# Optimization experiments

Measured on AMD Instinct MI355X. Metric: run time of the kernel, lower is better.

## Reference

```python
import jax, jax.numpy as jnp
import numpy as np

N, E, IN_DIM, H, D = 100000, 1600000, 256, 4, 32


def setup_inputs() -> dict:
    key = jax.random.key(0)
    ks = jax.random.split(key, 12)
    glorot = lambda k, shp: jax.random.normal(k, shp, dtype=jnp.float32) * np.float32(np.sqrt(2.0 / (shp[0] + shp[1])))
    return {
        "x": jax.random.normal(ks[0], (N, IN_DIM), dtype=jnp.float32),
        "row": jnp.sort(jax.random.randint(ks[1], (E,), 0, N)),
        "col": jax.random.randint(ks[2], (E,), 0, N),
        "a1_w": glorot(ks[3], (H, IN_DIM)),
        "a1_b": jnp.zeros((H,), jnp.float32),
        "a2_w": glorot(ks[4], (H, IN_DIM)),
        "a2_b": jnp.zeros((H,), jnp.float32),
        "lin_l_w": glorot(ks[5], (H * D, IN_DIM)),
        "lin_l_b": jnp.zeros((H * D,), jnp.float32),
        "lin_r_w": glorot(ks[6], (H * D, IN_DIM)),
        "lin_r_b": jnp.zeros((H * D,), jnp.float32),
    }


def reference(x, row, col, a1_w, a1_b, a2_w, a2_b, lin_l_w, lin_l_b, lin_r_w, lin_r_b):
    n = x.shape[0]
    # per-node attention logits, gathered per edge: attn[e,h] = a1(x)[row[e],h] + a2(x)[col[e],h]
    attn1 = x @ a1_w.T + a1_b            # [N, H]
    attn2 = x @ a2_w.T + a2_b            # [N, H]
    attn = attn1[row] + attn2[col]       # [E, H]
    # segment softmax over destination node (row), numerically stable
    seg_max = jax.ops.segment_max(attn, row, num_segments=n)
    seg_max = jnp.where(jnp.isfinite(seg_max), seg_max, 0.0)  # isolated nodes
    e = jnp.exp(attn - seg_max[row])
    seg_sum = jax.ops.segment_sum(e, row, num_segments=n)
    attn_d = e / (seg_sum[row] + 1e-16)  # [E, H]
    # per-head sparse weighted aggregation: out[r] += attn_d[e] * xw[col[e]]
    xw = (x @ lin_l_w.T + lin_l_b).reshape(n, H, D)
    msg = attn_d[:, :, None] * xw[col]   # [E, H, D]
    out_l = jax.ops.segment_sum(msg, row, num_segments=n).reshape(n, H * D)
    return out_l + x @ lin_r_w.T + lin_r_b
```

## Files before the change

### kernel.cpp

```cpp
#include <hip/hip_runtime.h>
#include <hip/hip_bf16.h>
#include <math.h>

#define IN_DIM 256
#define NH 4
#define HD 128

typedef __attribute__((ext_vector_type(8))) short short8;
typedef __attribute__((ext_vector_type(4))) float floatx4;
typedef __attribute__((ext_vector_type(2))) float floatx2;

__device__ __forceinline__ unsigned short f2bf(float f) {
    __hip_bfloat16 h = __float2bfloat16(f);
    return *reinterpret_cast<unsigned short*>(&h);
}
__device__ __forceinline__ float asf(unsigned int u) {
    union { unsigned int i; float f; } c; c.i = u; return c.f;
}

__global__ __launch_bounds__(256) void build_rowptr_k(const int* __restrict__ row,
                                                      int* __restrict__ rowptr,
                                                      int E, int N) {
    int e = blockIdx.x * blockDim.x + threadIdx.x;
    if (e >= E) return;
    int r = row[e];
    int rprev = (e > 0) ? row[e - 1] : -1;
    for (int rr = rprev + 1; rr <= r; ++rr) rowptr[rr] = e;
    if (e == E - 1) {
        for (int rr = r + 1; rr <= N; ++rr) rowptr[rr] = E;
    }
}

__global__ __launch_bounds__(256) void prep_w_k(const float* __restrict__ ll_w,
                                                const float* __restrict__ lr_w,
                                                unsigned short* __restrict__ Wb) {
    int idx = blockIdx.x * 256 + threadIdx.x;
    int j = idx >> 8, k = idx & 255;
    float v = (j < 128) ? ll_w[(size_t)j * 256 + k] : lr_w[(size_t)(j - 128) * 256 + k];
    Wb[idx] = f2bf(v);
}

__global__ __launch_bounds__(256) void attn_conv_k(
    const float* __restrict__ x,
    const float* __restrict__ a2_w, const float* __restrict__ a2_b,
    float* __restrict__ eattn, unsigned short* __restrict__ xb, int N)
{
    const int n = blockIdx.x * 4 + (threadIdx.x >> 6);
    const int lane = threadIdx.x & 63;
    if (n >= N) return;
    const float4 xv = ((const float4*)x)[(size_t)n * 64 + lane];
    ushort4 pk;
    pk.x = f2bf(xv.x); pk.y = f2bf(xv.y); pk.z = f2bf(xv.z); pk.w = f2bf(xv.w);
    *(ushort4*)(xb + (size_t)n * IN_DIM + lane * 4) = pk;
    #pragma unroll
    for (int c = 0; c < 4; ++c) {
        const float4 wv = ((const float4*)(a2_w + (size_t)c * IN_DIM))[lane];
        float p = xv.x * wv.x + xv.y * wv.y + xv.z * wv.z + xv.w * wv.w;
        #pragma unroll
        for (int o = 32; o; o >>= 1) p += __shfl_xor(p, o, 64);
        if (lane == 0) eattn[(size_t)n * NH + c] = __expf(p + a2_b[c]);
    }
}

__global__ __launch_bounds__(512, 4) void node_gemm_k(
    const unsigned short* __restrict__ xb, const unsigned short* __restrict__ Wb,
    const float* __restrict__ ll_b, const float* __restrict__ lr_b,
    unsigned short* __restrict__ xwb, float* __restrict__ out, int N)
{
    __shared__ unsigned short Abuf[2][32 * 264];
    __shared__ unsigned short LdsX[32 * 136];
    __shared__ float          LdsO[32 * 132];

    const int tid = threadIdx.x;
    const int lane = tid & 63;
    const int w = tid >> 6;
    const int lo = lane & 15;
    const int hi = lane >> 4;

    short8 Bf[2][8];
    int cols[2]; float bias[2];
    #pragma unroll
    for (int ct = 0; ct < 2; ++ct) {
        const int col = w * 32 + ct * 16 + lo;
        cols[ct] = col;
        bias[ct] = (col < HD) ? ll_b[col] : lr_b[col - HD];
        #pragma unroll
        for (int s = 0; s < 8; ++s)
            Bf[ct][s] = *(const short8*)(Wb + (size_t)col * IN_DIM + s * 32 + hi * 8);
    }

    const int tr = tid >> 4;
    const int tk = (tid & 15) * 16;

    uint4 st0, st1;
    auto gload = [&](int slab) {
        int rg = slab * 32 + tr;
        if (rg >= N) rg = 0;
        const uint4* p = (const uint4*)(xb + (size_t)rg * IN_DIM + tk);
        st0 = p[0]; st1 = p[1];
    };

    const int nslab = (N + 31) >> 5;
    int slab = blockIdx.x;
    gload(slab);
    int pb = 0;

    for (; slab < nslab; slab += gridDim.x) {
        unsigned short* ab = &Abuf[pb][0];
        *(uint4*)(ab + tr * 264 + tk) = st0;
        *(uint4*)(ab + tr * 264 + tk + 8) = st1;
        __syncthreads();

        const int next = slab + gridDim.x;
        if (next < nslab) gload(next);

        floatx4 acc[2][2];
        #pragma unroll
        for (int rt = 0; rt < 2; ++rt)
            #pragma unroll
            for (int ct = 0; ct < 2; ++ct)
                acc[rt][ct] = (floatx4){0.f, 0.f, 0.f, 0.f};

        #pragma unroll
        for (int s = 0; s < 8; ++s) {
            const short8 A0 = *(const short8*)(ab + lo * 264 + s * 32 + hi * 8);
            const short8 A1 = *(const short8*)(ab + (16 + lo) * 264 + s * 32 + hi * 8);
            acc[0][0] = __builtin_amdgcn_mfma_f32_16x16x32_bf16(A0, Bf[0][s], acc[0][0], 0, 0, 0);
            acc[0][1] = __builtin_amdgcn_mfma_f32_16x16x32_bf16(A0, Bf[1][s], acc[0][1], 0, 0, 0);
            acc[1][0] = __builtin_amdgcn_mfma_f32_16x16x32_bf16(A1, Bf[0][s], acc[1][0], 0, 0, 0);
            acc[1][1] = __builtin_amdgcn_mfma_f32_16x16x32_bf16(A1, Bf[1][s], acc[1][1], 0, 0, 0);
        }

        #pragma unroll
        for (int rt = 0; rt < 2; ++rt)
            #pragma unroll
            for (int ct = 0; ct < 2; ++ct) {
                const int c = cols[ct];
                #pragma unroll
                for (int j = 0; j < 4; ++j) {
                    const int r = rt * 16 + hi * 4 + j;
                    const float v = acc[rt][ct][j] + bias[ct];
                    if (c < HD) LdsX[r * 136 + c] = f2bf(v);
                    else        LdsO[r * 132 + (c - HD)] = v;
                }
            }

        asm volatile("s_waitcnt lgkmcnt(0)\n\ts_barrier" ::: "memory");

        {
            const int rg = slab * 32 + tr;
            if (rg < N) {
                *(uint4*)(xwb + (size_t)rg * HD + (tid & 15) * 8) =
                    *(const uint4*)(LdsX + tr * 136 + (tid & 15) * 8);
                float4* od = (float4*)(out + (size_t)rg * HD + (tid & 15) * 8);
                const float* lsrc = LdsO + tr * 132 + (tid & 15) * 8;
                od[0] = *(const float4*)(lsrc);
                od[1] = *(const float4*)(lsrc + 4);
            }
        }
        pb ^= 1;
    }
}

__global__ __launch_bounds__(256) void edge_aggregate_k(
    const int* __restrict__ rowptr, const int* __restrict__ col,
    const float* __restrict__ eattn,
    const unsigned short* __restrict__ xwb, float* __restrict__ out, int N)
{
    const int n = blockIdx.x * 4 + (threadIdx.x >> 6);
    const int lane = threadIdx.x & 63;
    if (n >= N) return;
    const int e0 = __builtin_amdgcn_readfirstlane(rowptr[n]);
    const int e1 = __builtin_amdgcn_readfirstlane(rowptr[n + 1]);
    if (e0 >= e1) return;

    const int h = lane >> 4;
    const int d2 = 2 * lane;

    floatx2* op = (floatx2*)(out + (size_t)n * HD + d2);
    floatx2 o = __builtin_nontemporal_load(op);

    float s = 0.f, acc0 = 0.f, acc1 = 0.f;
    int e = e0;

    if (e + 4 <= e1) {
        int c0 = col[e], c1 = col[e + 1], c2 = col[e + 2], c3 = col[e + 3];
        for (; e + 8 <= e1; e += 4) {
            const float w0 = eattn[c0 * NH + h];
            const float w1 = eattn[c1 * NH + h];
            const float w2 = eattn[c2 * NH + h];
            const float w3 = eattn[c3 * NH + h];
            const unsigned int p0 = *(const unsigned int*)(xwb + c0 * HD + d2);
            const unsigned int p1 = *(const unsigned int*)(xwb + c1 * HD + d2);
            const unsigned int p2 = *(const unsigned int*)(xwb + c2 * HD + d2);
            const unsigned int p3 = *(const unsigned int*)(xwb + c3 * HD + d2);
            const int n0 = col[e + 4];
            const int n1 = col[e + 5];
            const int n2 = col[e + 6];
            const int n3 = col[e + 7];
            s += (w0 + w1) + (w2 + w3);
            acc0 += w0 * asf(p0 << 16) + w1 * asf(p1 << 16);
            acc0 += w2 * asf(p2 << 16) + w3 * asf(p3 << 16);
            acc1 += w0 * asf(p0 & 0xffff0000u) + w1 * asf(p1 & 0xffff0000u);
            acc1 += w2 * asf(p2 & 0xffff0000u) + w3 * asf(p3 & 0xffff0000u);
            c0 = n0; c1 = n1; c2 = n2; c3 = n3;
        }
        {
            const float w0 = eattn[c0 * NH + h];
            const float w1 = eattn[c1 * NH + h];
            const float w2 = eattn[c2 * NH + h];
            const float w3 = eattn[c3 * NH + h];
            const unsigned int p0 = *(const unsigned int*)(xwb + c0 * HD + d2);
            const unsigned int p1 = *(const unsigned int*)(xwb + c1 * HD + d2);
            const unsigned int p2 = *(const unsigned int*)(xwb + c2 * HD + d2);
            const unsigned int p3 = *(const unsigned int*)(xwb + c3 * HD + d2);
            s += (w0 + w1) + (w2 + w3);
            acc0 += w0 * asf(p0 << 16) + w1 * asf(p1 << 16);
            acc0 += w2 * asf(p2 << 16) + w3 * asf(p3 << 16);
            acc1 += w0 * asf(p0 & 0xffff0000u) + w1 * asf(p1 & 0xffff0000u);
            acc1 += w2 * asf(p2 & 0xffff0000u) + w3 * asf(p3 & 0xffff0000u);
            e += 4;
        }
    }
    for (; e < e1; ++e) {
        const int c0 = col[e];
        const float w0 = eattn[c0 * NH + h];
        const unsigned int p0 = *(const unsigned int*)(xwb + c0 * HD + d2);
        s += w0;
        acc0 += w0 * asf(p0 << 16);
        acc1 += w0 * asf(p0 & 0xffff0000u);
    }

    const float inv = 1.f / s;
    o.x += acc0 * inv;
    o.y += acc1 * inv;
    __builtin_nontemporal_store(o, op);
}

extern "C" void kernel_launch(void* const* d_in, const int* in_sizes, int n_in,
                              void* d_out, int out_size, void* d_ws, size_t ws_size,
                              hipStream_t stream) {
    const float* x    = (const float*)d_in[0];
    const int*   row  = (const int*)d_in[1];
    const int*   col  = (const int*)d_in[2];
    const float* a2_w = (const float*)d_in[5];
    const float* a2_b = (const float*)d_in[6];
    const float* ll_w = (const float*)d_in[7];
    const float* ll_b = (const float*)d_in[8];
    const float* lr_w = (const float*)d_in[9];
    const float* lr_b = (const float*)d_in[10];
    float* out = (float*)d_out;

    const int N = in_sizes[0] / IN_DIM;
    const int E = in_sizes[1];

    char* ws = (char*)d_ws;
    size_t off = ((size_t)(N + 1) * sizeof(int) + 255) & ~(size_t)255;
    int*   rowptr = (int*)ws;
    float* eattn  = (float*)(ws + off); off += (size_t)N * NH * sizeof(float);
    unsigned short* xwb = (unsigned short*)(ws + off); off += (size_t)N * HD * sizeof(unsigned short);
    unsigned short* Wb  = (unsigned short*)(ws + off); off += (size_t)256 * IN_DIM * sizeof(unsigned short);
    unsigned short* xb  = (unsigned short*)(ws + off); off += (size_t)N * IN_DIM * sizeof(unsigned short);

    prep_w_k<<<256, 256, 0, stream>>>(ll_w, lr_w, Wb);
    build_rowptr_k<<<(E + 255) / 256, 256, 0, stream>>>(row, rowptr, E, N);
    attn_conv_k<<<(N + 3) / 4, 256, 0, stream>>>(x, a2_w, a2_b, eattn, xb, N);
    node_gemm_k<<<512, 512, 0, stream>>>(xb, Wb, ll_b, lr_b, xwb, out, N);
    edge_aggregate_k<<<(N + 3) / 4, 256, 0, stream>>>(rowptr, col, eattn, xwb, out, N);
}
```

Baseline: 309.4 us.

## Fuse bf16 conversion and attention logits into node GEMM; branchless edge loop

Removes the separate attn_conv kernel. The node GEMM now reads fp32 x directly, converts it to bf16 into LDS, and computes the a2 attention logits and their exponentials in-register with a 16-lane shuffle reduction. This drops the write and reread of the bf16 copy of x and one kernel launch, at the cost of more register pressure and ALU work inside the GEMM loop. The edge aggregation loop is also rewritten as a single masked 4-wide loop with clamped column prefetch, replacing the unrolled body plus scalar tail.

```diff
diff --git a/kernel.cpp b/kernel.cpp
--- a/kernel.cpp
+++ b/kernel.cpp
@@ -40,31 +40,11 @@
     Wb[idx] = f2bf(v);
 }
 
-__global__ __launch_bounds__(256) void attn_conv_k(
-    const float* __restrict__ x,
+__global__ __launch_bounds__(512, 4) void node_gemm_k(
+    const float* __restrict__ x, const unsigned short* __restrict__ Wb,
+    const float* __restrict__ ll_b, const float* __restrict__ lr_b,
     const float* __restrict__ a2_w, const float* __restrict__ a2_b,
-    float* __restrict__ eattn, unsigned short* __restrict__ xb, int N)
-{
-    const int n = blockIdx.x * 4 + (threadIdx.x >> 6);
-    const int lane = threadIdx.x & 63;
-    if (n >= N) return;
-    const float4 xv = ((const float4*)x)[(size_t)n * 64 + lane];
-    ushort4 pk;
-    pk.x = f2bf(xv.x); pk.y = f2bf(xv.y); pk.z = f2bf(xv.z); pk.w = f2bf(xv.w);
-    *(ushort4*)(xb + (size_t)n * IN_DIM + lane * 4) = pk;
-    #pragma unroll
-    for (int c = 0; c < 4; ++c) {
-        const float4 wv = ((const float4*)(a2_w + (size_t)c * IN_DIM))[lane];
-        float p = xv.x * wv.x + xv.y * wv.y + xv.z * wv.z + xv.w * wv.w;
-        #pragma unroll
-        for (int o = 32; o; o >>= 1) p += __shfl_xor(p, o, 64);
-        if (lane == 0) eattn[(size_t)n * NH + c] = __expf(p + a2_b[c]);
-    }
-}
-
-__global__ __launch_bounds__(512, 4) void node_gemm_k(
-    const unsigned short* __restrict__ xb, const unsigned short* __restrict__ Wb,
-    const float* __restrict__ ll_b, const float* __restrict__ lr_b,
+    float* __restrict__ eattn,
     unsigned short* __restrict__ xwb, float* __restrict__ out, int N)
 {
     __shared__ unsigned short Abuf[2][32 * 264];
@@ -90,29 +70,81 @@
     }
 
     const int tr = tid >> 4;
-    const int tk = (tid & 15) * 16;
-
-    uint4 st0, st1;
-    auto gload = [&](int slab) {
+    const int tq = tid & 15;
+
+    const float ab0 = a2_b[0], ab1 = a2_b[1], ab2 = a2_b[2], ab3 = a2_b[3];
+
+    float4 f0, f1, f2, f3;
+    auto gprefetch = [&](int slab) {
         int rg = slab * 32 + tr;
         if (rg >= N) rg = 0;
-        const uint4* p = (const uint4*)(xb + (size_t)rg * IN_DIM + tk);
-        st0 = p[0]; st1 = p[1];
+        const float* px = x + (size_t)rg * IN_DIM + tq * 4;
+        f0 = *(const float4*)(px);
+        f1 = *(const float4*)(px + 64);
+        f2 = *(const float4*)(px + 128);
+        f3 = *(const float4*)(px + 192);
     };
 
     const int nslab = (N + 31) >> 5;
     int slab = blockIdx.x;
-    gload(slab);
+    gprefetch(slab);
     int pb = 0;
 
     for (; slab < nslab; slab += gridDim.x) {
         unsigned short* ab = &Abuf[pb][0];
-        *(uint4*)(ab + tr * 264 + tk) = st0;
-        *(uint4*)(ab + tr * 264 + tk + 8) = st1;
-        __syncthreads();
+
+        {
+            ushort4 u;
+            u.x = f2bf(f0.x); u.y = f2bf(f0.y); u.z = f2bf(f0.z); u.w = f2bf(f0.w);
+            *(ushort4*)(ab + tr * 264 + tq * 4) = u;
+            u.x = f2bf(f1.x); u.y = f2bf(f1.y); u.z = f2bf(f1.z); u.w = f2bf(f1.w);
+            *(ushort4*)(ab + tr * 264 + 64 + tq * 4) = u;
+            u.x = f2bf(f2.x); u.y = f2bf(f2.y); u.z = f2bf(f2.z); u.w = f2bf(f2.w);
+            *(ushort4*)(ab + tr * 264 + 128 + tq * 4) = u;
+            u.x = f2bf(f3.x); u.y = f2bf(f3.y); u.z = f2bf(f3.z); u.w = f2bf(f3.w);
+            *(ushort4*)(ab + tr * 264 + 192 + tq * 4) = u;
+        }
+
+        float p0 = 0.f, p1 = 0.f, p2 = 0.f, p3 = 0.f;
+        {
+            const float* aw = a2_w + tq * 4;
+            #pragma unroll
+            for (int j = 0; j < 4; ++j) {
+                const float4 fx = (j == 0) ? f0 : (j == 1) ? f1 : (j == 2) ? f2 : f3;
+                const float4 w0v = *(const float4*)(aw + 0 * IN_DIM + j * 64);
+                const float4 w1v = *(const float4*)(aw + 1 * IN_DIM + j * 64);
+                const float4 w2v = *(const float4*)(aw + 2 * IN_DIM + j * 64);
+                const float4 w3v = *(const float4*)(aw + 3 * IN_DIM + j * 64);
+                p0 += fx.x * w0v.x + fx.y * w0v.y + fx.z * w0v.z + fx.w * w0v.w;
+                p1 += fx.x * w1v.x + fx.y * w1v.y + fx.z * w1v.z + fx.w * w1v.w;
+                p2 += fx.x * w2v.x + fx.y * w2v.y + fx.z * w2v.z + fx.w * w2v.w;
+                p3 += fx.x * w3v.x + fx.y * w3v.y + fx.z * w3v.z + fx.w * w3v.w;
+            }
+        }
+
+        asm volatile("s_waitcnt lgkmcnt(0)\n\ts_barrier" ::: "memory");
+
+        #pragma unroll
+        for (int o = 1; o < 16; o <<= 1) {
+            p0 += __shfl_xor(p0, o, 64);
+            p1 += __shfl_xor(p1, o, 64);
+            p2 += __shfl_xor(p2, o, 64);
+            p3 += __shfl_xor(p3, o, 64);
+        }
+        {
+            const int rgo = slab * 32 + tr;
+            if (tq == 0 && rgo < N) {
+                float4 ev;
+                ev.x = __expf(p0 + ab0);
+                ev.y = __expf(p1 + ab1);
+                ev.z = __expf(p2 + ab2);
+                ev.w = __expf(p3 + ab3);
+                *(float4*)(eattn + (size_t)rgo * NH) = ev;
+            }
+        }
 
         const int next = slab + gridDim.x;
-        if (next < nslab) gload(next);
+        if (next < nslab) gprefetch(next);
 
         floatx4 acc[2][2];
         #pragma unroll
@@ -150,10 +182,10 @@
         {
             const int rg = slab * 32 + tr;
             if (rg < N) {
-                *(uint4*)(xwb + (size_t)rg * HD + (tid & 15) * 8) =
-                    *(const uint4*)(LdsX + tr * 136 + (tid & 15) * 8);
-                float4* od = (float4*)(out + (size_t)rg * HD + (tid & 15) * 8);
-                const float* lsrc = LdsO + tr * 132 + (tid & 15) * 8;
+                *(uint4*)(xwb + (size_t)rg * HD + tq * 8) =
+                    *(const uint4*)(LdsX + tr * 136 + tq * 8);
+                float4* od = (float4*)(out + (size_t)rg * HD + tq * 8);
+                const float* lsrc = LdsO + tr * 132 + tq * 8;
                 od[0] = *(const float4*)(lsrc);
                 od[1] = *(const float4*)(lsrc + 4);
             }
@@ -165,7 +197,8 @@
 __global__ __launch_bounds__(256) void edge_aggregate_k(
     const int* __restrict__ rowptr, const int* __restrict__ col,
     const float* __restrict__ eattn,
-    const unsigned short* __restrict__ xwb, float* __restrict__ out, int N)
+    const unsigned short* __restrict__ xwb, float* __restrict__ out,
+    int N, int E)
 {
     const int n = blockIdx.x * 4 + (threadIdx.x >> 6);
     const int lane = threadIdx.x & 63;
@@ -176,59 +209,38 @@
 
     const int h = lane >> 4;
     const int d2 = 2 * lane;
+    const int elast = E - 1;
+
+    auto cl = [&](int i) { return col[i <= elast ? i : elast]; };
 
     floatx2* op = (floatx2*)(out + (size_t)n * HD + d2);
     floatx2 o = __builtin_nontemporal_load(op);
 
     float s = 0.f, acc0 = 0.f, acc1 = 0.f;
     int e = e0;
-
-    if (e + 4 <= e1) {
-        int c0 = col[e], c1 = col[e + 1], c2 = col[e + 2], c3 = col[e + 3];
-        for (; e + 8 <= e1; e += 4) {
-            const float w0 = eattn[c0 * NH + h];
-            const float w1 = eattn[c1 * NH + h];
-            const float w2 = eattn[c2 * NH + h];
-            const float w3 = eattn[c3 * NH + h];
-            const unsigned int p0 = *(const unsigned int*)(xwb + c0 * HD + d2);
-            const unsigned int p1 = *(const unsigned int*)(xwb + c1 * HD + d2);
-            const unsigned int p2 = *(const unsigned int*)(xwb + c2 * HD + d2);
-            const unsigned int p3 = *(const unsigned int*)(xwb + c3 * HD + d2);
-            const int n0 = col[e + 4];
-            const int n1 = col[e + 5];
-            const int n2 = col[e + 6];
-            const int n3 = col[e + 7];
-            s += (w0 + w1) + (w2 + w3);
-            acc0 += w0 * asf(p0 << 16) + w1 * asf(p1 << 16);
-            acc0 += w2 * asf(p2 << 16) + w3 * asf(p3 << 16);
-            acc1 += w0 * asf(p0 & 0xffff0000u) + w1 * asf(p1 & 0xffff0000u);
-            acc1 += w2 * asf(p2 & 0xffff0000u) + w3 * asf(p3 & 0xffff0000u);
-            c0 = n0; c1 = n1; c2 = n2; c3 = n3;
-        }
-        {
-            const float w0 = eattn[c0 * NH + h];
-            const float w1 = eattn[c1 * NH + h];
-            const float w2 = eattn[c2 * NH + h];
-            const float w3 = eattn[c3 * NH + h];
-            const unsigned int p0 = *(const unsigned int*)(xwb + c0 * HD + d2);
-            const unsigned int p1 = *(const unsigned int*)(xwb + c1 * HD + d2);
-            const unsigned int p2 = *(const unsigned int*)(xwb + c2 * HD + d2);
-            const unsigned int p3 = *(const unsigned int*)(xwb + c3 * HD + d2);
-            s += (w0 + w1) + (w2 + w3);
-            acc0 += w0 * asf(p0 << 16) + w1 * asf(p1 << 16);
-            acc0 += w2 * asf(p2 << 16) + w3 * asf(p3 << 16);
-            acc1 += w0 * asf(p0 & 0xffff0000u) + w1 * asf(p1 & 0xffff0000u);
-            acc1 += w2 * asf(p2 & 0xffff0000u) + w3 * asf(p3 & 0xffff0000u);
-            e += 4;
-        }
-    }
-    for (; e < e1; ++e) {
-        const int c0 = col[e];
-        const float w0 = eattn[c0 * NH + h];
-        const unsigned int p0 = *(const unsigned int*)(xwb + c0 * HD + d2);
-        s += w0;
-        acc0 += w0 * asf(p0 << 16);
-        acc1 += w0 * asf(p0 & 0xffff0000u);
+    int c0 = cl(e), c1 = cl(e + 1), c2 = cl(e + 2), c3 = cl(e + 3);
+
+    for (;;) {
+        float w0 = eattn[c0 * NH + h];
+        float w1 = eattn[c1 * NH + h];
+        float w2 = eattn[c2 * NH + h];
+        float w3 = eattn[c3 * NH + h];
+        const unsigned int p0 = *(const unsigned int*)(xwb + (size_t)c0 * HD + d2);
+        const unsigned int p1 = *(const unsigned int*)(xwb + (size_t)c1 * HD + d2);
+        const unsigned int p2 = *(const unsigned int*)(xwb + (size_t)c2 * HD + d2);
+        const unsigned int p3 = *(const unsigned int*)(xwb + (size_t)c3 * HD + d2);
+        const int ne = e + 4;
+        const int n0 = cl(ne), n1 = cl(ne + 1), n2 = cl(ne + 2), n3 = cl(ne + 3);
+        w1 = (e + 1 < e1) ? w1 : 0.f;
+        w2 = (e + 2 < e1) ? w2 : 0.f;
+        w3 = (e + 3 < e1) ? w3 : 0.f;
+        s += (w0 + w1) + (w2 + w3);
+        acc0 += w0 * asf(p0 << 16) + w1 * asf(p1 << 16);
+        acc0 += w2 * asf(p2 << 16) + w3 * asf(p3 << 16);
+        acc1 += w0 * asf(p0 & 0xffff0000u) + w1 * asf(p1 & 0xffff0000u);
+        acc1 += w2 * asf(p2 & 0xffff0000u) + w3 * asf(p3 & 0xffff0000u);
+        if (ne >= e1) break;
+        e = ne; c0 = n0; c1 = n1; c2 = n2; c3 = n3;
     }
 
     const float inv = 1.f / s;
@@ -260,11 +272,9 @@
     float* eattn  = (float*)(ws + off); off += (size_t)N * NH * sizeof(float);
     unsigned short* xwb = (unsigned short*)(ws + off); off += (size_t)N * HD * sizeof(unsigned short);
     unsigned short* Wb  = (unsigned short*)(ws + off); off += (size_t)256 * IN_DIM * sizeof(unsigned short);
-    unsigned short* xb  = (unsigned short*)(ws + off); off += (size_t)N * IN_DIM * sizeof(unsigned short);
 
     prep_w_k<<<256, 256, 0, stream>>>(ll_w, lr_w, Wb);
     build_rowptr_k<<<(E + 255) / 256, 256, 0, stream>>>(row, rowptr, E, N);
-    attn_conv_k<<<(N + 3) / 4, 256, 0, stream>>>(x, a2_w, a2_b, eattn, xb, N);
-    node_gemm_k<<<512, 512, 0, stream>>>(xb, Wb, ll_b, lr_b, xwb, out, N);
-    edge_aggregate_k<<<(N + 3) / 4, 256, 0, stream>>>(rowptr, col, eattn, xwb, out, N);
-}
+    node_gemm_k<<<512, 512, 0, stream>>>(x, Wb, ll_b, lr_b, a2_w, a2_b, eattn, xwb, out, N);
+    edge_aggregate_k<<<(N + 3) / 4, 256, 0, stream>>>(rowptr, col, eattn, xwb, out, N, E);
+}
```

Result: slower. 349.3 us (+12.9%).
